# Performance work log

Measured on AMD Instinct MI355X. Metric: run time of the kernel, lower is better.

## Reference

```python
import jax, jax.numpy as jnp
import numpy as np

N_NODES = 100000
N_EDGES = 1600000
IN_DIM = 48
HID = 16
N_CLASSES = 8


def _sage_conv(x, src, dst, W_l, W_r, b, n_nodes):
    # PyG SAGEConv (aggr='mean', root_weight=True):
    #   out_i = W_l @ mean_{j in N(i)} x_j + b + W_r @ x_i
    msg = x[src]                                              # [E, F]
    agg = jax.ops.segment_sum(msg, dst, num_segments=n_nodes)  # [N, F]
    deg = jax.ops.segment_sum(jnp.ones((src.shape[0],), x.dtype), dst,
                              num_segments=n_nodes)            # [N]
    agg = agg / jnp.maximum(deg, 1.0)[:, None]
    return agg @ W_l.T + b + x @ W_r.T


def setup_inputs() -> dict:
    key = jax.random.key(0)
    ks = jax.random.split(key, 10)
    def lin(k, out_d, in_d):
        s = 1.0 / np.sqrt(in_d)
        return jax.random.uniform(k, (out_d, in_d), jnp.float32, -s, s)
    x = jax.random.normal(ks[0], (N_NODES, IN_DIM), jnp.float32)
    edge_index = jax.random.randint(ks[1], (2, N_EDGES), 0, N_NODES, jnp.int64)
    return {
        "x": x,
        "edge_index": edge_index,
        "W1_l": lin(ks[2], HID, IN_DIM), "W1_r": lin(ks[3], HID, IN_DIM),
        "b1": jnp.zeros((HID,), jnp.float32),
        "W2_l": lin(ks[4], HID, HID), "W2_r": lin(ks[5], HID, HID),
        "b2": jnp.zeros((HID,), jnp.float32),
        "W3_l": lin(ks[6], N_CLASSES, HID), "W3_r": lin(ks[7], N_CLASSES, HID),
        "b3": jnp.zeros((N_CLASSES,), jnp.float32),
    }


def reference(x, edge_index, W1_l, W1_r, b1, W2_l, W2_r, b2, W3_l, W3_r, b3):
    src, dst = edge_index[0], edge_index[1]
    n = x.shape[0]
    # dropout is identity in deterministic/eval reference
    h = jax.nn.elu(_sage_conv(x, src, dst, W1_l, W1_r, b1, n))
    h = jax.nn.elu(_sage_conv(h, src, dst, W2_l, W2_r, b2, n))
    h = jax.nn.elu(_sage_conv(h, src, dst, W3_l, W3_r, b3, n))
    return jax.nn.log_softmax(h, axis=-1)
```

## Files before the change

### kernel.cpp

```cpp
#include <hip/hip_runtime.h>
#include <hip/hip_bf16.h>
#include <math.h>

#define N_IN   48
#define N_HID  16
#define N_CLS  8
#define CAP    48
#define NB_SHIFT 9
#define TILE   4096
#define CAPB   9216
#define WSTR   52

__device__ __forceinline__ float bf2f(unsigned short u) {
    union { unsigned int i; float f; } c;
    c.i = ((unsigned int)u) << 16;
    return c.f;
}
__device__ __forceinline__ unsigned short f2bf(float f) {
    unsigned int u = __float_as_uint(f);
    unsigned int r = u + 0x7FFFu + ((u >> 16) & 1u);
    return (unsigned short)(r >> 16);
}

__device__ __forceinline__ void acc16(const ushort4* __restrict__ P4, int mul, int q,
        int4 a0, int4 a1, int4 a2, int4 a3, float4& acc) {
    ushort4 t0 = P4[(size_t)a0.x * mul + q];
    ushort4 t1 = P4[(size_t)a0.y * mul + q];
    ushort4 t2 = P4[(size_t)a0.z * mul + q];
    ushort4 t3 = P4[(size_t)a0.w * mul + q];
    ushort4 t4 = P4[(size_t)a1.x * mul + q];
    ushort4 t5 = P4[(size_t)a1.y * mul + q];
    ushort4 t6 = P4[(size_t)a1.z * mul + q];
    ushort4 t7 = P4[(size_t)a1.w * mul + q];
    ushort4 t8 = P4[(size_t)a2.x * mul + q];
    ushort4 t9 = P4[(size_t)a2.y * mul + q];
    ushort4 ta = P4[(size_t)a2.z * mul + q];
    ushort4 tb = P4[(size_t)a2.w * mul + q];
    ushort4 tc = P4[(size_t)a3.x * mul + q];
    ushort4 td = P4[(size_t)a3.y * mul + q];
    ushort4 te = P4[(size_t)a3.z * mul + q];
    ushort4 tf = P4[(size_t)a3.w * mul + q];
    acc.x += ((((bf2f(t0.x)+bf2f(t1.x))+(bf2f(t2.x)+bf2f(t3.x)))
             + ((bf2f(t4.x)+bf2f(t5.x))+(bf2f(t6.x)+bf2f(t7.x))))
            + (((bf2f(t8.x)+bf2f(t9.x))+(bf2f(ta.x)+bf2f(tb.x)))
             + ((bf2f(tc.x)+bf2f(td.x))+(bf2f(te.x)+bf2f(tf.x)))));
    acc.y += ((((bf2f(t0.y)+bf2f(t1.y))+(bf2f(t2.y)+bf2f(t3.y)))
             + ((bf2f(t4.y)+bf2f(t5.y))+(bf2f(t6.y)+bf2f(t7.y))))
            + (((bf2f(t8.y)+bf2f(t9.y))+(bf2f(ta.y)+bf2f(tb.y)))
             + ((bf2f(tc.y)+bf2f(td.y))+(bf2f(te.y)+bf2f(tf.y)))));
    acc.z += ((((bf2f(t0.z)+bf2f(t1.z))+(bf2f(t2.z)+bf2f(t3.z)))
             + ((bf2f(t4.z)+bf2f(t5.z))+(bf2f(t6.z)+bf2f(t7.z))))
            + (((bf2f(t8.z)+bf2f(t9.z))+(bf2f(ta.z)+bf2f(tb.z)))
             + ((bf2f(tc.z)+bf2f(td.z))+(bf2f(te.z)+bf2f(tf.z)))));
    acc.w += ((((bf2f(t0.w)+bf2f(t1.w))+(bf2f(t2.w)+bf2f(t3.w)))
             + ((bf2f(t4.w)+bf2f(t5.w))+(bf2f(t6.w)+bf2f(t7.w))))
            + (((bf2f(t8.w)+bf2f(t9.w))+(bf2f(ta.w)+bf2f(tb.w)))
             + ((bf2f(tc.w)+bf2f(td.w))+(bf2f(te.w)+bf2f(tf.w)))));
}

__global__ __launch_bounds__(256) void scatter_tiles_kernel(
        const int* __restrict__ src, const int* __restrict__ dst,
        int* __restrict__ cursor, int* __restrict__ ebuf, int E) {
    __shared__ int lh[256];
    __shared__ int gbase[256];
    __shared__ int rank[256];
    int t = threadIdx.x;
    lh[t] = 0;
    rank[t] = 0;
    __syncthreads();
    int base = blockIdx.x * TILE;
    int dcache[TILE / 256];
#pragma unroll
    for (int k = 0; k < TILE / 256; k++) {
        int e = base + t + k * 256;
        dcache[k] = -1;
        if (e < E) {
            int d = dst[e];
            dcache[k] = d;
            atomicAdd(&lh[d >> NB_SHIFT], 1);
        }
    }
    __syncthreads();
    if (lh[t]) gbase[t] = atomicAdd(&cursor[t], lh[t]);
    __syncthreads();
#pragma unroll
    for (int k = 0; k < TILE / 256; k++) {
        int e = base + t + k * 256;
        if (e < E) {
            int d = dcache[k];
            int b = d >> NB_SHIFT;
            int r = gbase[b] + atomicAdd(&rank[b], 1);
            if (r < CAPB)
                ebuf[b * CAPB + r] = ((d & 511) << 17) | src[e];
        }
    }
}

__global__ __launch_bounds__(256) void fill_proj_kernel(
        const int* __restrict__ cursor, const int* __restrict__ ebuf,
        int* __restrict__ cnt, int* __restrict__ adj,
        const float* __restrict__ X,
        const float* __restrict__ Wl, const float* __restrict__ Wr,
        const float* __restrict__ b,
        unsigned short* __restrict__ P, unsigned short* __restrict__ S,
        int N, int nbuck) {
    __shared__ int   lc[512];
    __shared__ float sWl[N_HID * WSTR];
    __shared__ float sWr[N_HID * WSTR];
    __shared__ float sb[N_HID];
    int t = threadIdx.x;

    if ((int)blockIdx.x < nbuck) {
        int bb = blockIdx.x;
        int nodeBeg = bb << NB_SHIFT;
        for (int i = t; i < 512; i += 256) lc[i] = 0;
        __syncthreads();
        int nb = cursor[bb];
        if (nb > CAPB) nb = CAPB;
        int beg = bb * CAPB, end = beg + nb;
        for (int e = beg + t; e < end; e += 256) {
            int v = ebuf[e];
            int ld = ((unsigned int)v) >> 17;
            int s  = v & 0x1FFFF;
            int p = atomicAdd(&lc[ld], 1);
            if (p < CAP) adj[(size_t)(nodeBeg + ld) * CAP + p] = s;
        }
        __syncthreads();
        for (int i = t; i < 512; i += 256) {
            int node = nodeBeg + i;
            if (node >= N) continue;
            int c = lc[i];
            cnt[node] = c;
            if (c > CAP) c = CAP;
            int degp = (c + 15) & ~15;
            if (degp < 16) degp = 16;
            int* row = adj + (size_t)node * CAP;
            for (int p = c; p < degp; p++) row[p] = N;
        }
        return;
    }

    for (int idx = t; idx < N_HID * N_IN; idx += 256) {
        int r = idx / N_IN, k = idx - r * N_IN;
        sWl[r * WSTR + k] = Wl[idx];
        sWr[r * WSTR + k] = Wr[idx];
    }
    if (t < N_HID) sb[t] = b[t];
    __syncthreads();

    int node = ((int)blockIdx.x - nbuck) * 64 + (t >> 2);
    int q = t & 3;
    if (node > N) return;
    int gid = node * 4 + q;
    if (node == N) {
        reinterpret_cast<ushort4*>(P)[gid] = make_ushort4(0, 0, 0, 0);
        reinterpret_cast<ushort4*>(S)[gid] = make_ushort4(0, 0, 0, 0);
        return;
    }

    const float4* xrow = reinterpret_cast<const float4*>(X + (size_t)node * N_IN);
    float accL[4], accR[4];
#pragma unroll
    for (int oo = 0; oo < 4; oo++) { accL[oo] = 0.0f; accR[oo] = sb[4 * q + oo]; }

#pragma unroll
    for (int c = 0; c < N_IN / 4; c++) {
        float4 xv = xrow[c];
#pragma unroll
        for (int oo = 0; oo < 4; oo++) {
            int row = 4 * q + oo;
            float4 wl = *reinterpret_cast<const float4*>(&sWl[row * WSTR + 4 * c]);
            float4 wr = *reinterpret_cast<const float4*>(&sWr[row * WSTR + 4 * c]);
            accL[oo] = fmaf(xv.x, wl.x, accL[oo]); accR[oo] = fmaf(xv.x, wr.x, accR[oo]);
            accL[oo] = fmaf(xv.y, wl.y, accL[oo]); accR[oo] = fmaf(xv.y, wr.y, accR[oo]);
            accL[oo] = fmaf(xv.z, wl.z, accL[oo]); accR[oo] = fmaf(xv.z, wr.z, accR[oo]);
            accL[oo] = fmaf(xv.w, wl.w, accL[oo]); accR[oo] = fmaf(xv.w, wr.w, accR[oo]);
        }
    }

    reinterpret_cast<ushort4*>(P)[gid] =
        make_ushort4(f2bf(accL[0]), f2bf(accL[1]), f2bf(accL[2]), f2bf(accL[3]));
    reinterpret_cast<ushort4*>(S)[gid] =
        make_ushort4(f2bf(accR[0]), f2bf(accR[1]), f2bf(accR[2]), f2bf(accR[3]));
}

__global__ __launch_bounds__(256) void gather_proj16_kernel(
        const int* __restrict__ cnt, const int* __restrict__ adj,
        const unsigned short* __restrict__ Pin, const unsigned short* __restrict__ Sin,
        const float* __restrict__ Wl, const float* __restrict__ Wr,
        const float* __restrict__ bias,
        unsigned short* __restrict__ Pout, unsigned short* __restrict__ Sout, int N) {
    int gid = blockIdx.x * blockDim.x + threadIdx.x;
    if (gid >= N * 4) return;
    if (gid < 4)
        reinterpret_cast<ushort4*>(Pout)[(size_t)N * 4 + gid] = make_ushort4(0, 0, 0, 0);
    int i = gid >> 2;
    int q = gid & 3;
    int deg = cnt[i];
    if (deg > CAP) deg = CAP;
    int degp = (deg + 15) & ~15;
    if (degp < 16) degp = 16;
    const int4* lst4 = reinterpret_cast<const int4*>(adj + (size_t)i * CAP);
    int4 a0 = lst4[0], a1 = lst4[1], a2 = lst4[2], a3 = lst4[3];
    int4 b0 = lst4[4], b1 = lst4[5], b2 = lst4[6], b3 = lst4[7];
    ushort4 svu = reinterpret_cast<const ushort4*>(Sin)[gid];
    const ushort4* P4 = reinterpret_cast<const ushort4*>(Pin);
    float4 acc = make_float4(0.f, 0.f, 0.f, 0.f);
    acc16(P4, 4, q, a0, a1, a2, a3, acc);
    if (degp > 16) {
        acc16(P4, 4, q, b0, b1, b2, b3, acc);
        if (degp > 32)
            acc16(P4, 4, q, lst4[8], lst4[9], lst4[10], lst4[11], acc);
    }
    float inv = 1.0f / (float)max(deg, 1);
    float4 h;
    h.x = acc.x * inv + bf2f(svu.x); h.y = acc.y * inv + bf2f(svu.y);
    h.z = acc.z * inv + bf2f(svu.z); h.w = acc.w * inv + bf2f(svu.w);
    h.x = h.x > 0.f ? h.x : expm1f(h.x);
    h.y = h.y > 0.f ? h.y : expm1f(h.y);
    h.z = h.z > 0.f ? h.z : expm1f(h.z);
    h.w = h.w > 0.f ? h.w : expm1f(h.w);

    int lane = threadIdx.x & 63;
    int lb = lane & ~3;
    float hv[16];
#pragma unroll
    for (int a = 0; a < 4; a++) {
        hv[4 * a + 0] = __shfl(h.x, lb + a, 64);
        hv[4 * a + 1] = __shfl(h.y, lb + a, 64);
        hv[4 * a + 2] = __shfl(h.z, lb + a, 64);
        hv[4 * a + 3] = __shfl(h.w, lb + a, 64);
    }

    const float4* Wl4 = reinterpret_cast<const float4*>(Wl);
    const float4* Wr4 = reinterpret_cast<const float4*>(Wr);
    float pl[4], sr[4];
#pragma unroll
    for (int oo = 0; oo < 4; oo++) {
        int o = 4 * q + oo;
        float aL = 0.0f, aR = bias[o];
#pragma unroll
        for (int c = 0; c < 4; c++) {
            float4 wl = Wl4[o * 4 + c];
            float4 wr = Wr4[o * 4 + c];
            aL = fmaf(hv[4 * c + 0], wl.x, aL); aR = fmaf(hv[4 * c + 0], wr.x, aR);
            aL = fmaf(hv[4 * c + 1], wl.y, aL); aR = fmaf(hv[4 * c + 1], wr.y, aR);
            aL = fmaf(hv[4 * c + 2], wl.z, aL); aR = fmaf(hv[4 * c + 2], wr.z, aR);
            aL = fmaf(hv[4 * c + 3], wl.w, aL); aR = fmaf(hv[4 * c + 3], wr.w, aR);
        }
        pl[oo] = aL; sr[oo] = aR;
    }
    reinterpret_cast<ushort4*>(Pout)[gid] =
        make_ushort4(f2bf(pl[0]), f2bf(pl[1]), f2bf(pl[2]), f2bf(pl[3]));
    reinterpret_cast<ushort4*>(Sout)[gid] =
        make_ushort4(f2bf(sr[0]), f2bf(sr[1]), f2bf(sr[2]), f2bf(sr[3]));
}

__global__ __launch_bounds__(256) void gather_proj8_kernel(
        const int* __restrict__ cnt, const int* __restrict__ adj,
        const unsigned short* __restrict__ Pin, const unsigned short* __restrict__ Sin,
        const float* __restrict__ Wl, const float* __restrict__ Wr,
        const float* __restrict__ bias,
        unsigned int* __restrict__ Pout, unsigned int* __restrict__ Sout, int N) {
    int gid = blockIdx.x * blockDim.x + threadIdx.x;
    if (gid >= N * 4) return;
    if (gid < 4)
        Pout[(size_t)N * 4 + gid] = 0u;
    int i = gid >> 2;
    int q = gid & 3;
    int deg = cnt[i];
    if (deg > CAP) deg = CAP;
    int degp = (deg + 15) & ~15;
    if (degp < 16) degp = 16;
    const int4* lst4 = reinterpret_cast<const int4*>(adj + (size_t)i * CAP);
    int4 a0 = lst4[0], a1 = lst4[1], a2 = lst4[2], a3 = lst4[3];
    int4 b0 = lst4[4], b1 = lst4[5], b2 = lst4[6], b3 = lst4[7];
    ushort4 svu = reinterpret_cast<const ushort4*>(Sin)[gid];
    const ushort4* P4 = reinterpret_cast<const ushort4*>(Pin);
    float4 acc = make_float4(0.f, 0.f, 0.f, 0.f);
    acc16(P4, 4, q, a0, a1, a2, a3, acc);
    if (degp > 16) {
        acc16(P4, 4, q, b0, b1, b2, b3, acc);
        if (degp > 32)
            acc16(P4, 4, q, lst4[8], lst4[9], lst4[10], lst4[11], acc);
    }
    float inv = 1.0f / (float)max(deg, 1);
    float4 h;
    h.x = acc.x * inv + bf2f(svu.x); h.y = acc.y * inv + bf2f(svu.y);
    h.z = acc.z * inv + bf2f(svu.z); h.w = acc.w * inv + bf2f(svu.w);
    h.x = h.x > 0.f ? h.x : expm1f(h.x);
    h.y = h.y > 0.f ? h.y : expm1f(h.y);
    h.z = h.z > 0.f ? h.z : expm1f(h.z);
    h.w = h.w > 0.f ? h.w : expm1f(h.w);

    int lane = threadIdx.x & 63;
    int lb = lane & ~3;
    float hv[16];
#pragma unroll
    for (int a = 0; a < 4; a++) {
        hv[4 * a + 0] = __shfl(h.x, lb + a, 64);
        hv[4 * a + 1] = __shfl(h.y, lb + a, 64);
        hv[4 * a + 2] = __shfl(h.z, lb + a, 64);
        hv[4 * a + 3] = __shfl(h.w, lb + a, 64);
    }

    const float4* Wl4 = reinterpret_cast<const float4*>(Wl);
    const float4* Wr4 = reinterpret_cast<const float4*>(Wr);
    float pl[2], sr[2];
#pragma unroll
    for (int oo = 0; oo < 2; oo++) {
        int o = 2 * q + oo;
        float aL = 0.0f, aR = bias[o];
#pragma unroll
        for (int c = 0; c < 4; c++) {
            float4 wl = Wl4[o * 4 + c];
            float4 wr = Wr4[o * 4 + c];
            aL = fmaf(hv[4 * c + 0], wl.x, aL); aR = fmaf(hv[4 * c + 0], wr.x, aR);
            aL = fmaf(hv[4 * c + 1], wl.y, aL); aR = fmaf(hv[4 * c + 1], wr.y, aR);
            aL = fmaf(hv[4 * c + 2], wl.z, aL); aR = fmaf(hv[4 * c + 2], wr.z, aR);
            aL = fmaf(hv[4 * c + 3], wl.w, aL); aR = fmaf(hv[4 * c + 3], wr.w, aR);
        }
        pl[oo] = aL; sr[oo] = aR;
    }
    Pout[gid] = ((unsigned int)f2bf(pl[1]) << 16) | f2bf(pl[0]);
    Sout[gid] = ((unsigned int)f2bf(sr[1]) << 16) | f2bf(sr[0]);
}

__global__ __launch_bounds__(256) void gather8_kernel(
        const int* __restrict__ cnt, const int* __restrict__ adj,
        const unsigned short* __restrict__ P, const unsigned short* __restrict__ S,
        float* __restrict__ out, int N) {
    int gid = blockIdx.x * blockDim.x + threadIdx.x;
    if (gid >= N * 2) return;
    int i = gid >> 1;
    int q = gid & 1;
    int deg = cnt[i];
    if (deg > CAP) deg = CAP;
    int degp = (deg + 15) & ~15;
    if (degp < 16) degp = 16;
    const int4* lst4 = reinterpret_cast<const int4*>(adj + (size_t)i * CAP);
    int4 a0 = lst4[0], a1 = lst4[1], a2 = lst4[2], a3 = lst4[3];
    int4 b0 = lst4[4], b1 = lst4[5], b2 = lst4[6], b3 = lst4[7];
    ushort4 svu = reinterpret_cast<const ushort4*>(S)[gid];
    const ushort4* P4 = reinterpret_cast<const ushort4*>(P);
    float4 acc = make_float4(0.f, 0.f, 0.f, 0.f);
    acc16(P4, 2, q, a0, a1, a2, a3, acc);
    if (degp > 16) {
        acc16(P4, 2, q, b0, b1, b2, b3, acc);
        if (degp > 32)
            acc16(P4, 2, q, lst4[8], lst4[9], lst4[10], lst4[11], acc);
    }
    float inv = 1.0f / (float)max(deg, 1);
    float4 v;
    v.x = acc.x * inv + bf2f(svu.x); v.y = acc.y * inv + bf2f(svu.y);
    v.z = acc.z * inv + bf2f(svu.z); v.w = acc.w * inv + bf2f(svu.w);
    v.x = v.x > 0.f ? v.x : expm1f(v.x);
    v.y = v.y > 0.f ? v.y : expm1f(v.y);
    v.z = v.z > 0.f ? v.z : expm1f(v.z);
    v.w = v.w > 0.f ? v.w : expm1f(v.w);
    float m = fmaxf(fmaxf(v.x, v.y), fmaxf(v.z, v.w));
    m = fmaxf(m, __shfl_xor(m, 1));
    float sum = expf(v.x - m) + expf(v.y - m) + expf(v.z - m) + expf(v.w - m);
    sum += __shfl_xor(sum, 1);
    float lse = m + logf(sum);
    reinterpret_cast<float4*>(out)[gid] =
        make_float4(v.x - lse, v.y - lse, v.z - lse, v.w - lse);
}

extern "C" void kernel_launch(void* const* d_in, const int* in_sizes, int n_in,
                              void* d_out, int out_size, void* d_ws, size_t ws_size,
                              hipStream_t stream) {
    const float* x   = (const float*)d_in[0];
    const int*   ei  = (const int*)d_in[1];
    const float* W1l = (const float*)d_in[2];
    const float* W1r = (const float*)d_in[3];
    const float* b1  = (const float*)d_in[4];
    const float* W2l = (const float*)d_in[5];
    const float* W2r = (const float*)d_in[6];
    const float* b2  = (const float*)d_in[7];
    const float* W3l = (const float*)d_in[8];
    const float* W3r = (const float*)d_in[9];
    const float* b3  = (const float*)d_in[10];
    float* out = (float*)d_out;

    const int N = in_sizes[0] / N_IN;
    const int E = in_sizes[1] / 2;
    const int* src = ei;
    const int* dst = ei + E;
    const int nbuck = (N + 511) >> NB_SHIFT;

    int* cursor = (int*)d_ws;
    int* cnt    = cursor + 256;
    int  Npad   = (N + 3) & ~3;
    int* adj    = cnt + Npad;
    int* ebuf   = adj + (size_t)N * CAP;
    const size_t Nr = (size_t)N + 1;
    unsigned short* P1 = (unsigned short*)(ebuf + (size_t)nbuck * CAPB);
    unsigned short* P2 = P1 + Nr * N_HID;
    unsigned short* S1 = P2 + Nr * N_HID;
    unsigned short* S3 = S1 + Nr * N_HID;
    unsigned short* P3 = P1;

    hipMemsetAsync(cursor, 0, 256 * sizeof(int), stream);

    const int B = 256;
    int n4Grid   = (N * 4 + B - 1) / B;
    int n2Grid   = (N * 2 + B - 1) / B;
    int p1Grid   = (N + 1 + 63) / 64;
    int tileGrid = (E + TILE - 1) / TILE;

    scatter_tiles_kernel<<<tileGrid, B, 0, stream>>>(src, dst, cursor, ebuf, E);

    fill_proj_kernel<<<nbuck + p1Grid, B, 0, stream>>>(
        cursor, ebuf, cnt, adj, x, W1l, W1r, b1, P1, S1, N, nbuck);

    gather_proj16_kernel<<<n4Grid, B, 0, stream>>>(cnt, adj, P1, S1,
                                                   W2l, W2r, b2, P2, S1, N);

    gather_proj8_kernel<<<n4Grid, B, 0, stream>>>(cnt, adj, P2, S1,
                                                  W3l, W3r, b3,
                                                  (unsigned int*)P3,
                                                  (unsigned int*)S3, N);

    gather8_kernel<<<n2Grid, B, 0, stream>>>(cnt, adj, P3, S3, out, N);
}
```

Measured before the change: 213.0 us.

## Split final gather across two thread halves and use 32-bit indexing

The last layer's gather now runs four threads per node instead of two. Each half takes half of the neighbor list, and the partial sums are combined with a cross-lane shuffle, which doubles the memory-level parallelism for the gather-bound final layer. Index arithmetic across all gather kernels switches from 64-bit size_t to unsigned 32-bit, and the second adjacency block is loaded only when the degree needs it. Launch bounds ask for an occupancy of 6 blocks, which may push the compiler toward register spills.

```diff
diff --git a/kernel.cpp b/kernel.cpp
--- a/kernel.cpp
+++ b/kernel.cpp
@@ -22,24 +22,25 @@
     return (unsigned short)(r >> 16);
 }
 
-__device__ __forceinline__ void acc16(const ushort4* __restrict__ P4, int mul, int q,
+__device__ __forceinline__ void acc16(const ushort4* __restrict__ P4,
+        unsigned mul, unsigned q,
         int4 a0, int4 a1, int4 a2, int4 a3, float4& acc) {
-    ushort4 t0 = P4[(size_t)a0.x * mul + q];
-    ushort4 t1 = P4[(size_t)a0.y * mul + q];
-    ushort4 t2 = P4[(size_t)a0.z * mul + q];
-    ushort4 t3 = P4[(size_t)a0.w * mul + q];
-    ushort4 t4 = P4[(size_t)a1.x * mul + q];
-    ushort4 t5 = P4[(size_t)a1.y * mul + q];
-    ushort4 t6 = P4[(size_t)a1.z * mul + q];
-    ushort4 t7 = P4[(size_t)a1.w * mul + q];
-    ushort4 t8 = P4[(size_t)a2.x * mul + q];
-    ushort4 t9 = P4[(size_t)a2.y * mul + q];
-    ushort4 ta = P4[(size_t)a2.z * mul + q];
-    ushort4 tb = P4[(size_t)a2.w * mul + q];
-    ushort4 tc = P4[(size_t)a3.x * mul + q];
-    ushort4 td = P4[(size_t)a3.y * mul + q];
-    ushort4 te = P4[(size_t)a3.z * mul + q];
-    ushort4 tf = P4[(size_t)a3.w * mul + q];
+    ushort4 t0 = P4[(unsigned)a0.x * mul + q];
+    ushort4 t1 = P4[(unsigned)a0.y * mul + q];
+    ushort4 t2 = P4[(unsigned)a0.z * mul + q];
+    ushort4 t3 = P4[(unsigned)a0.w * mul + q];
+    ushort4 t4 = P4[(unsigned)a1.x * mul + q];
+    ushort4 t5 = P4[(unsigned)a1.y * mul + q];
+    ushort4 t6 = P4[(unsigned)a1.z * mul + q];
+    ushort4 t7 = P4[(unsigned)a1.w * mul + q];
+    ushort4 t8 = P4[(unsigned)a2.x * mul + q];
+    ushort4 t9 = P4[(unsigned)a2.y * mul + q];
+    ushort4 ta = P4[(unsigned)a2.z * mul + q];
+    ushort4 tb = P4[(unsigned)a2.w * mul + q];
+    ushort4 tc = P4[(unsigned)a3.x * mul + q];
+    ushort4 td = P4[(unsigned)a3.y * mul + q];
+    ushort4 te = P4[(unsigned)a3.z * mul + q];
+    ushort4 tf = P4[(unsigned)a3.w * mul + q];
     acc.x += ((((bf2f(t0.x)+bf2f(t1.x))+(bf2f(t2.x)+bf2f(t3.x)))
              + ((bf2f(t4.x)+bf2f(t5.x))+(bf2f(t6.x)+bf2f(t7.x))))
             + (((bf2f(t8.x)+bf2f(t9.x))+(bf2f(ta.x)+bf2f(tb.x)))
@@ -58,6 +59,27 @@
              + ((bf2f(tc.w)+bf2f(td.w))+(bf2f(te.w)+bf2f(tf.w)))));
 }
 
+__device__ __forceinline__ void acc8(const ushort4* __restrict__ P4,
+        unsigned mul, unsigned q,
+        int4 a0, int4 a1, float4& acc) {
+    ushort4 t0 = P4[(unsigned)a0.x * mul + q];
+    ushort4 t1 = P4[(unsigned)a0.y * mul + q];
+    ushort4 t2 = P4[(unsigned)a0.z * mul + q];
+    ushort4 t3 = P4[(unsigned)a0.w * mul + q];
+    ushort4 t4 = P4[(unsigned)a1.x * mul + q];
+    ushort4 t5 = P4[(unsigned)a1.y * mul + q];
+    ushort4 t6 = P4[(unsigned)a1.z * mul + q];
+    ushort4 t7 = P4[(unsigned)a1.w * mul + q];
+    acc.x += ((bf2f(t0.x)+bf2f(t1.x))+(bf2f(t2.x)+bf2f(t3.x)))
+           + ((bf2f(t4.x)+bf2f(t5.x))+(bf2f(t6.x)+bf2f(t7.x)));
+    acc.y += ((bf2f(t0.y)+bf2f(t1.y))+(bf2f(t2.y)+bf2f(t3.y)))
+           + ((bf2f(t4.y)+bf2f(t5.y))+(bf2f(t6.y)+bf2f(t7.y)));
+    acc.z += ((bf2f(t0.z)+bf2f(t1.z))+(bf2f(t2.z)+bf2f(t3.z)))
+           + ((bf2f(t4.z)+bf2f(t5.z))+(bf2f(t6.z)+bf2f(t7.z)));
+    acc.w += ((bf2f(t0.w)+bf2f(t1.w))+(bf2f(t2.w)+bf2f(t3.w)))
+           + ((bf2f(t4.w)+bf2f(t5.w))+(bf2f(t6.w)+bf2f(t7.w)));
+}
+
 __global__ __launch_bounds__(256) void scatter_tiles_kernel(
         const int* __restrict__ src, const int* __restrict__ dst,
         int* __restrict__ cursor, int* __restrict__ ebuf, int E) {
@@ -184,7 +206,7 @@
         make_ushort4(f2bf(accR[0]), f2bf(accR[1]), f2bf(accR[2]), f2bf(accR[3]));
 }
 
-__global__ __launch_bounds__(256) void gather_proj16_kernel(
+__global__ __launch_bounds__(256, 6) void gather_proj16_kernel(
         const int* __restrict__ cnt, const int* __restrict__ adj,
         const unsigned short* __restrict__ Pin, const unsigned short* __restrict__ Sin,
         const float* __restrict__ Wl, const float* __restrict__ Wr,
@@ -193,24 +215,25 @@
     int gid = blockIdx.x * blockDim.x + threadIdx.x;
     if (gid >= N * 4) return;
     if (gid < 4)
-        reinterpret_cast<ushort4*>(Pout)[(size_t)N * 4 + gid] = make_ushort4(0, 0, 0, 0);
+        reinterpret_cast<ushort4*>(Pout)[(unsigned)N * 4u + gid] = make_ushort4(0, 0, 0, 0);
     int i = gid >> 2;
-    int q = gid & 3;
+    unsigned q = gid & 3;
     int deg = cnt[i];
     if (deg > CAP) deg = CAP;
     int degp = (deg + 15) & ~15;
     if (degp < 16) degp = 16;
-    const int4* lst4 = reinterpret_cast<const int4*>(adj + (size_t)i * CAP);
+    const int4* lst4 = reinterpret_cast<const int4*>(adj) + (unsigned)i * (CAP / 4);
     int4 a0 = lst4[0], a1 = lst4[1], a2 = lst4[2], a3 = lst4[3];
-    int4 b0 = lst4[4], b1 = lst4[5], b2 = lst4[6], b3 = lst4[7];
-    ushort4 svu = reinterpret_cast<const ushort4*>(Sin)[gid];
+    ushort4 svu = reinterpret_cast<const ushort4*>(Sin)[(unsigned)gid];
     const ushort4* P4 = reinterpret_cast<const ushort4*>(Pin);
     float4 acc = make_float4(0.f, 0.f, 0.f, 0.f);
-    acc16(P4, 4, q, a0, a1, a2, a3, acc);
+    int4 b0, b1, b2, b3;
+    if (degp > 16) { b0 = lst4[4]; b1 = lst4[5]; b2 = lst4[6]; b3 = lst4[7]; }
+    acc16(P4, 4u, q, a0, a1, a2, a3, acc);
     if (degp > 16) {
-        acc16(P4, 4, q, b0, b1, b2, b3, acc);
+        acc16(P4, 4u, q, b0, b1, b2, b3, acc);
         if (degp > 32)
-            acc16(P4, 4, q, lst4[8], lst4[9], lst4[10], lst4[11], acc);
+            acc16(P4, 4u, q, lst4[8], lst4[9], lst4[10], lst4[11], acc);
     }
     float inv = 1.0f / (float)max(deg, 1);
     float4 h;
@@ -250,13 +273,13 @@
         }
         pl[oo] = aL; sr[oo] = aR;
     }
-    reinterpret_cast<ushort4*>(Pout)[gid] =
+    reinterpret_cast<ushort4*>(Pout)[(unsigned)gid] =
         make_ushort4(f2bf(pl[0]), f2bf(pl[1]), f2bf(pl[2]), f2bf(pl[3]));
-    reinterpret_cast<ushort4*>(Sout)[gid] =
+    reinterpret_cast<ushort4*>(Sout)[(unsigned)gid] =
         make_ushort4(f2bf(sr[0]), f2bf(sr[1]), f2bf(sr[2]), f2bf(sr[3]));
 }
 
-__global__ __launch_bounds__(256) void gather_proj8_kernel(
+__global__ __launch_bounds__(256, 6) void gather_proj8_kernel(
         const int* __restrict__ cnt, const int* __restrict__ adj,
         const unsigned short* __restrict__ Pin, const unsigned short* __restrict__ Sin,
         const float* __restrict__ Wl, const float* __restrict__ Wr,
@@ -265,24 +288,25 @@
     int gid = blockIdx.x * blockDim.x + threadIdx.x;
     if (gid >= N * 4) return;
     if (gid < 4)
-        Pout[(size_t)N * 4 + gid] = 0u;
+        Pout[(unsigned)N * 4u + gid] = 0u;
     int i = gid >> 2;
-    int q = gid & 3;
+    unsigned q = gid & 3;
     int deg = cnt[i];
     if (deg > CAP) deg = CAP;
     int degp = (deg + 15) & ~15;
     if (degp < 16) degp = 16;
-    const int4* lst4 = reinterpret_cast<const int4*>(adj + (size_t)i * CAP);
+    const int4* lst4 = reinterpret_cast<const int4*>(adj) + (unsigned)i * (CAP / 4);
     int4 a0 = lst4[0], a1 = lst4[1], a2 = lst4[2], a3 = lst4[3];
-    int4 b0 = lst4[4], b1 = lst4[5], b2 = lst4[6], b3 = lst4[7];
-    ushort4 svu = reinterpret_cast<const ushort4*>(Sin)[gid];
+    ushort4 svu = reinterpret_cast<const ushort4*>(Sin)[(unsigned)gid];
     const ushort4* P4 = reinterpret_cast<const ushort4*>(Pin);
     float4 acc = make_float4(0.f, 0.f, 0.f, 0.f);
-    acc16(P4, 4, q, a0, a1, a2, a3, acc);
+    int4 b0, b1, b2, b3;
+    if (degp > 16) { b0 = lst4[4]; b1 = lst4[5]; b2 = lst4[6]; b3 = lst4[7]; }
+    acc16(P4, 4u, q, a0, a1, a2, a3, acc);
     if (degp > 16) {
-        acc16(P4, 4, q, b0, b1, b2, b3, acc);
+        acc16(P4, 4u, q, b0, b1, b2, b3, acc);
         if (degp > 32)
-            acc16(P4, 4, q, lst4[8], lst4[9], lst4[10], lst4[11], acc);
+            acc16(P4, 4u, q, lst4[8], lst4[9], lst4[10], lst4[11], acc);
     }
     float inv = 1.0f / (float)max(deg, 1);
     float4 h;
@@ -322,34 +346,41 @@
         }
         pl[oo] = aL; sr[oo] = aR;
     }
-    Pout[gid] = ((unsigned int)f2bf(pl[1]) << 16) | f2bf(pl[0]);
-    Sout[gid] = ((unsigned int)f2bf(sr[1]) << 16) | f2bf(sr[0]);
-}
-
-__global__ __launch_bounds__(256) void gather8_kernel(
+    Pout[(unsigned)gid] = ((unsigned int)f2bf(pl[1]) << 16) | f2bf(pl[0]);
+    Sout[(unsigned)gid] = ((unsigned int)f2bf(sr[1]) << 16) | f2bf(sr[0]);
+}
+
+__global__ __launch_bounds__(256, 6) void gather8_kernel(
         const int* __restrict__ cnt, const int* __restrict__ adj,
         const unsigned short* __restrict__ P, const unsigned short* __restrict__ S,
         float* __restrict__ out, int N) {
-    int gid = blockIdx.x * blockDim.x + threadIdx.x;
-    if (gid >= N * 2) return;
-    int i = gid >> 1;
-    int q = gid & 1;
+    int t = blockIdx.x * blockDim.x + threadIdx.x;
+    if (t >= N * 4) return;
+    int i = t >> 2;
+    unsigned sub = t & 3;
+    unsigned q  = sub & 1;
+    unsigned hf = sub >> 1;
     int deg = cnt[i];
     if (deg > CAP) deg = CAP;
     int degp = (deg + 15) & ~15;
     if (degp < 16) degp = 16;
-    const int4* lst4 = reinterpret_cast<const int4*>(adj + (size_t)i * CAP);
-    int4 a0 = lst4[0], a1 = lst4[1], a2 = lst4[2], a3 = lst4[3];
-    int4 b0 = lst4[4], b1 = lst4[5], b2 = lst4[6], b3 = lst4[7];
-    ushort4 svu = reinterpret_cast<const ushort4*>(S)[gid];
+    const int4* lst4 = reinterpret_cast<const int4*>(adj) + (unsigned)i * (CAP / 4);
+    ushort4 svu = reinterpret_cast<const ushort4*>(S)[(unsigned)i * 2u + q];
     const ushort4* P4 = reinterpret_cast<const ushort4*>(P);
     float4 acc = make_float4(0.f, 0.f, 0.f, 0.f);
-    acc16(P4, 2, q, a0, a1, a2, a3, acc);
-    if (degp > 16) {
-        acc16(P4, 2, q, b0, b1, b2, b3, acc);
+    if (degp == 16) {
+        acc8(P4, 2u, q, lst4[hf * 2 + 0], lst4[hf * 2 + 1], acc);
+    } else {
+        acc16(P4, 2u, q, lst4[hf * 4 + 0], lst4[hf * 4 + 1],
+                          lst4[hf * 4 + 2], lst4[hf * 4 + 3], acc);
         if (degp > 32)
-            acc16(P4, 2, q, lst4[8], lst4[9], lst4[10], lst4[11], acc);
-    }
+            acc8(P4, 2u, q, lst4[8 + hf * 2], lst4[9 + hf * 2], acc);
+    }
+    acc.x += __shfl_xor(acc.x, 2, 64);
+    acc.y += __shfl_xor(acc.y, 2, 64);
+    acc.z += __shfl_xor(acc.z, 2, 64);
+    acc.w += __shfl_xor(acc.w, 2, 64);
+
     float inv = 1.0f / (float)max(deg, 1);
     float4 v;
     v.x = acc.x * inv + bf2f(svu.x); v.y = acc.y * inv + bf2f(svu.y);
@@ -359,12 +390,13 @@
     v.z = v.z > 0.f ? v.z : expm1f(v.z);
     v.w = v.w > 0.f ? v.w : expm1f(v.w);
     float m = fmaxf(fmaxf(v.x, v.y), fmaxf(v.z, v.w));
-    m = fmaxf(m, __shfl_xor(m, 1));
+    m = fmaxf(m, __shfl_xor(m, 1, 64));
     float sum = expf(v.x - m) + expf(v.y - m) + expf(v.z - m) + expf(v.w - m);
-    sum += __shfl_xor(sum, 1);
+    sum += __shfl_xor(sum, 1, 64);
     float lse = m + logf(sum);
-    reinterpret_cast<float4*>(out)[gid] =
-        make_float4(v.x - lse, v.y - lse, v.z - lse, v.w - lse);
+    if (hf == 0)
+        reinterpret_cast<float4*>(out)[(unsigned)i * 2u + q] =
+            make_float4(v.x - lse, v.y - lse, v.z - lse, v.w - lse);
 }
 
 extern "C" void kernel_launch(void* const* d_in, const int* in_sizes, int n_in,
@@ -405,7 +437,6 @@
 
     const int B = 256;
     int n4Grid   = (N * 4 + B - 1) / B;
-    int n2Grid   = (N * 2 + B - 1) / B;
     int p1Grid   = (N + 1 + 63) / 64;
     int tileGrid = (E + TILE - 1) / TILE;
 
@@ -422,5 +453,5 @@
                                                   (unsigned int*)P3,
                                                   (unsigned int*)S3, N);
 
-    gather8_kernel<<<n2Grid, B, 0, stream>>>(cnt, adj, P3, S3, out, N);
-}
+    gather8_kernel<<<n4Grid, B, 0, stream>>>(cnt, adj, P3, S3, out, N);
+}
```

Result: no change. 212.3 us (-0.3%).
